# Kernel optimization log

Hardware: AMD Instinct MI355X
Metric: run time of the kernel (lower is better)

## Reference

```python
import jax, jax.numpy as jnp
from jax import lax
import numpy as np

# pywt db4 decomposition filters (8 taps)
DEC_LO = np.array([-0.010597401785069032, 0.0328830116668852, 0.030841381835560764,
                   -0.18703481171909309, -0.027983769416859854, 0.6308807679298589,
                   0.7148465705529157, 0.2303778133088965], dtype=np.float32)
DEC_HI = np.array([-0.2303778133088965, 0.7148465705529157, -0.6308807679298589,
                   -0.027983769416859854, 0.18703481171909309, 0.030841381835560764,
                   -0.0328830116668852, -0.010597401785069032], dtype=np.float32)

LEVELS = 5
POOL = 128       # adaptive pool size inside each WaveletLevelNet
LEVEL_HID = 128  # per-level net output dim
OUT_DIM = 512
BATCH, SIGLEN = 2048, 16384


def dwt_step(a, filt):
    """One DWT level. a: [B, n]; filt: [2, L] (dec_lo, dec_hi).
    pywt-style: symmetric pad, full convolution, downsample at odd indices.
    Output length = floor((n + L - 1)/2)."""
    L = filt.shape[-1]
    xp = jnp.pad(a, ((0, 0), (L - 2, L - 1)), mode='symmetric')[:, None, :]  # [B,1,n+2L-3]
    k = filt[:, ::-1][:, None, :]  # flip -> true convolution; [2,1,L]
    out = lax.conv_general_dilated(xp, k, (2,), 'VALID',
                                   dimension_numbers=('NCH', 'OIH', 'NCH'))  # [B,2,m]
    return out[:, 0, :], out[:, 1, :]  # cA, cD


def wavedec(x, levels):
    filt = jnp.stack([jnp.asarray(DEC_LO), jnp.asarray(DEC_HI)])
    a = x
    details = []
    for _ in range(levels):  # small fixed loop over levels
        a, d = dwt_step(a, filt)
        details.append(d)
    return [a] + details[::-1]  # [cA_L, cD_L, cD_{L-1}, ..., cD_1]


def adaptive_avg_pool(x, P):
    """torch AdaptiveAvgPool1d over last dim via cumsum segment means."""
    n = x.shape[-1]
    idx = np.arange(P)
    starts = (idx * n) // P
    ends = ((idx + 1) * n + P - 1) // P
    cs = jnp.cumsum(x, axis=-1)
    cs = jnp.concatenate([jnp.zeros_like(cs[..., :1]), cs], axis=-1)
    return (cs[..., ends] - cs[..., starts]) / jnp.asarray(ends - starts, x.dtype)


def setup_inputs() -> dict:
    key = jax.random.key(0)
    k0, k1, k2 = jax.random.split(key, 3)
    x = jax.random.normal(k0, (BATCH, SIGLEN), dtype=jnp.float32)
    level_w = jax.random.normal(k1, (LEVELS, LEVEL_HID, POOL), dtype=jnp.float32) * 0.05
    level_b = jnp.zeros((LEVELS, LEVEL_HID), dtype=jnp.float32)
    fusion_w = jax.random.normal(k2, (OUT_DIM, LEVELS * LEVEL_HID), dtype=jnp.float32) * 0.05
    fusion_b = jnp.zeros((OUT_DIM,), dtype=jnp.float32)
    return {"x": x, "level_w": level_w, "level_b": level_b,
            "fusion_w": fusion_w, "fusion_b": fusion_b}


def reference(x, level_w, level_b, fusion_w, fusion_b):
    coeffs = wavedec(x, LEVELS)  # 6 arrays; forward uses the first 5
    pooled = jnp.stack([adaptive_avg_pool(coeffs[i], POOL) for i in range(LEVELS)])  # [5,B,P]
    feats = jax.nn.relu(jnp.einsum('lbp,lop->lbo', pooled, level_w) + level_b[:, None, :])
    comb = jnp.transpose(feats, (1, 0, 2)).reshape(x.shape[0], LEVELS * LEVEL_HID)  # [B,640]
    return jax.nn.relu(comb @ fusion_w.T + fusion_b)  # Dropout is identity in eval
```

## Files before the change

kernel.cpp:

```cpp
#include <hip/hip_runtime.h>


#define BATCH   2048
#define SIGLEN  16384
#define N1      8195
#define N2      4101
#define N3      2054
#define N4      1030
#define N5      518
#define POOLP   128
#define COMB    640
#define OUTD    512
#define NTHR    512

#define LW_PAIRS (5 * 128 * 128 / 2)
#define FW_PAIRS (512 * 640 / 2)
#define PACK_BLOCKS ((LW_PAIRS + FW_PAIRS) / 256)

#define SWZ(i) ((i) ^ ((((i) >> 5) & 7) << 2))

typedef __fp16 h2 __attribute__((ext_vector_type(2)));
typedef float  f2 __attribute__((ext_vector_type(2)));

__device__ constexpr float LO[8] = {
     0.2303778133088965f,   0.7148465705529157f,   0.6308807679298589f,
    -0.027983769416859854f, -0.18703481171909309f,  0.030841381835560764f,
     0.0328830116668852f,  -0.010597401785069032f };
__device__ constexpr float HI[8] = {
    -0.010597401785069032f, -0.0328830116668852f,   0.030841381835560764f,
     0.18703481171909309f,  -0.027983769416859854f, -0.6308807679298589f,
     0.7148465705529157f,  -0.2303778133088965f };

__device__ __forceinline__ int symfold(int idx, int n) {
    idx = (idx < 0) ? (-1 - idx) : idx;
    idx = (idx >= n) ? (2 * n - 1 - idx) : idx;
    return idx;
}
constexpr int cmin(int a, int b) { return a < b ? a : b; }
constexpr int cmax(int a, int b) { return a > b ? a : b; }

template<int SS, int SE, int BSRC, int NSRC, int S, int E, int BDST>
__device__ __forceinline__ void dwt_chunk(const float* __restrict__ src,
                                          float* __restrict__ dstA,
                                          float* __restrict__ dstD, int tid) {
    for (int j0 = (S & ~3) + tid * 4; j0 < E; j0 += NTHR * 4) {
        const int rb = 2 * j0 - 8;
        if ((rb >= SS) && (2 * j0 + 7 <= SE - 1) && (j0 + 4 <= E)) {
            const int lrb = rb - BSRC;
            const float4 v0 = *reinterpret_cast<const float4*>(src + SWZ(lrb));
            const float4 v1 = *reinterpret_cast<const float4*>(src + SWZ(lrb + 4));
            const float4 v2 = *reinterpret_cast<const float4*>(src + SWZ(lrb + 8));
            const float4 v3 = *reinterpret_cast<const float4*>(src + SWZ(lrb + 12));
            float w[16];
            w[0]=v0.x;  w[1]=v0.y;  w[2]=v0.z;  w[3]=v0.w;
            w[4]=v1.x;  w[5]=v1.y;  w[6]=v1.z;  w[7]=v1.w;
            w[8]=v2.x;  w[9]=v2.y;  w[10]=v2.z; w[11]=v2.w;
            w[12]=v3.x; w[13]=v3.y; w[14]=v3.z; w[15]=v3.w;
            float a[4], d[4];
#pragma unroll
            for (int k = 0; k < 4; ++k) {
                f2 ad = {0.f, 0.f};
#pragma unroll
                for (int t = 0; t < 8; ++t) {
                    const float v = w[2 + 2 * k + t];
                    const f2 vv = {v, v};
                    const f2 lh = {LO[t], HI[t]};
                    ad = __builtin_elementwise_fma(vv, lh, ad);
                }
                a[k] = ad.x; d[k] = ad.y;
            }
            const int ds = j0 - BDST;
            *reinterpret_cast<float4*>(dstA + SWZ(ds)) = make_float4(a[0], a[1], a[2], a[3]);
            *reinterpret_cast<float4*>(dstD + SWZ(ds)) = make_float4(d[0], d[1], d[2], d[3]);
        } else {
            for (int k = 0; k < 4; ++k) {
                const int j = j0 + k;
                if (j < S || j >= E) continue;
                float aa = 0.f, dd = 0.f;
#pragma unroll
                for (int t = 0; t < 8; ++t) {
                    const int idx = symfold(2 * j - 6 + t, NSRC);
                    const float v = src[SWZ(idx - BSRC)];
                    aa = fmaf(v, LO[t], aa);
                    dd = fmaf(v, HI[t], dd);
                }
                dstA[SWZ(j - BDST)] = aa;
                dstD[SWZ(j - BDST)] = dd;
            }
        }
    }
}

template<int S, int E, int BDST>
__device__ __forceinline__ void dwt_l1(const float* __restrict__ xr,
                                       float* __restrict__ dstA, int tid) {
    for (int j0 = (S & ~3) + tid * 4; j0 < E; j0 += NTHR * 4) {
        const int rb = 2 * j0 - 8;
        if ((rb >= 0) && (2 * j0 + 7 <= SIGLEN - 1) && (j0 + 4 <= E)) {
            const float4* s4 = reinterpret_cast<const float4*>(xr + rb);
            const float4 v0 = s4[0], v1 = s4[1], v2 = s4[2], v3 = s4[3];
            float w[16];
            w[0]=v0.x;  w[1]=v0.y;  w[2]=v0.z;  w[3]=v0.w;
            w[4]=v1.x;  w[5]=v1.y;  w[6]=v1.z;  w[7]=v1.w;
            w[8]=v2.x;  w[9]=v2.y;  w[10]=v2.z; w[11]=v2.w;
            w[12]=v3.x; w[13]=v3.y; w[14]=v3.z; w[15]=v3.w;
            f2 a01 = {0.f, 0.f}, a23 = {0.f, 0.f};
#pragma unroll
            for (int t = 0; t < 8; ++t) {
                const f2 p01 = {w[2 + t], w[4 + t]};
                const f2 p23 = {w[6 + t], w[8 + t]};
                const f2 lt  = {LO[t], LO[t]};
                a01 = __builtin_elementwise_fma(p01, lt, a01);
                a23 = __builtin_elementwise_fma(p23, lt, a23);
            }
            *reinterpret_cast<float4*>(dstA + SWZ(j0 - BDST)) =
                make_float4(a01.x, a01.y, a23.x, a23.y);
        } else {
            for (int k = 0; k < 4; ++k) {
                const int j = j0 + k;
                if (j < S || j >= E) continue;
                float aa = 0.f;
#pragma unroll
                for (int t = 0; t < 8; ++t) {
                    const int idx = symfold(2 * j - 6 + t, SIGLEN);
                    aa = fmaf(xr[idx], LO[t], aa);
                }
                dstA[SWZ(j - BDST)] = aa;
            }
        }
    }
}

template<int N, int BASE, int P0>
__device__ __forceinline__ void pool64(const float* __restrict__ buf,
                                       __fp16* __restrict__ dst, int tid) {
    const int p = P0 + (tid >> 3), sub = tid & 7;
    const int s = (p * N) >> 7;
    const int e = ((p + 1) * N + 127) >> 7;
    float acc = 0.f;
    for (int t = s + sub; t < e; t += 8) acc += buf[SWZ(t - BASE)];
    acc += __shfl_xor(acc, 1);
    acc += __shfl_xor(acc, 2);
    acc += __shfl_xor(acc, 4);
    if (sub == 0) dst[p] = (__fp16)(acc / (float)(e - s));
}

template<int B>
__device__ __forceinline__ void dwt_body(const float* __restrict__ xr,
                                         __fp16* __restrict__ pr,
                                         float* __restrict__ A, float* __restrict__ Bb,
                                         float* __restrict__ D1, float* __restrict__ D2,
                                         int tid) {
    constexpr int p0 = B * 64;
    constexpr int sP5 = (p0 * N5) >> 7, eP5 = ((p0 + 64) * N5 + 127) >> 7;
    constexpr int sP4 = (p0 * N4) >> 7, eP4 = ((p0 + 64) * N4 + 127) >> 7;
    constexpr int sP3 = (p0 * N3) >> 7, eP3 = ((p0 + 64) * N3 + 127) >> 7;
    constexpr int sP2 = (p0 * N2) >> 7, eP2 = ((p0 + 64) * N2 + 127) >> 7;
    constexpr int s5 = sP5, e5 = cmin(eP5, N5);
    constexpr int s4 = cmax(cmin(sP4, 2 * s5 - 6), 0);
    constexpr int e4 = cmin(cmax(eP4, 2 * e5), N4);
    constexpr int s3 = cmax(cmin(sP3, 2 * s4 - 6), 0);
    constexpr int e3 = cmin(cmax(eP3, 2 * e4), N3);
    constexpr int s2 = cmax(cmin(sP2, 2 * s3 - 6), 0);
    constexpr int e2 = cmin(cmax(eP2, 2 * e3), N2);
    constexpr int s1 = cmax(2 * s2 - 6, 0);
    constexpr int e1 = cmin(2 * e2, N1);
    constexpr int b1 = (s1 & ~3) - 8, b2 = (s2 & ~3) - 8, b3 = (s3 & ~3) - 8;
    constexpr int b4 = (s4 & ~3) - 8, b5 = (s5 & ~3) - 8;

    dwt_l1<s1, e1, b1>(xr, A, tid);
    __syncthreads();
    dwt_chunk<s1, e1, b1, N1, s2, e2, b2>(A, Bb, D1, tid);
    __syncthreads();
    dwt_chunk<s2, e2, b2, N2, s3, e3, b3>(Bb, A, D2, tid);
    pool64<N2, b2, p0>(D1, pr + 4 * POOLP, tid);
    __syncthreads();
    dwt_chunk<s3, e3, b3, N3, s4, e4, b4>(A, Bb, D1, tid);
    pool64<N3, b3, p0>(D2, pr + 3 * POOLP, tid);
    __syncthreads();
    dwt_chunk<s4, e4, b4, N4, s5, e5, b5>(Bb, A, D2, tid);
    pool64<N4, b4, p0>(D1, pr + 2 * POOLP, tid);
    __syncthreads();
    pool64<N5, b5, p0>(A,  pr + 0 * POOLP, tid);
    pool64<N5, b5, p0>(D2, pr + 1 * POOLP, tid);
}

__global__ __launch_bounds__(NTHR, 4) void dwt_pool_kernel(const float* __restrict__ x,
                                                           __fp16* __restrict__ pooled,
                                                           const float* __restrict__ lw,
                                                           const float* __restrict__ fw,
                                                           h2* __restrict__ lwh,
                                                           h2* __restrict__ fwh) {
    __shared__ __align__(16) float A[4192];
    __shared__ __align__(16) float Bb[2144];
    __shared__ __align__(16) float D1[2144];
    __shared__ __align__(16) float D2[1088];
    const int tid = threadIdx.x;

    if (lwh != nullptr && blockIdx.x < PACK_BLOCKS && tid < 256) {
        const int i = blockIdx.x * 256 + tid;
        if (i < LW_PAIRS) {
            const float2 v = reinterpret_cast<const float2*>(lw)[i];
            lwh[i] = __builtin_amdgcn_cvt_pkrtz(v.x, v.y);
        } else {
            const float2 v = reinterpret_cast<const float2*>(fw)[i - LW_PAIRS];
            fwh[i - LW_PAIRS] = __builtin_amdgcn_cvt_pkrtz(v.x, v.y);
        }
    }

    const int row = blockIdx.x >> 1;
    const float* __restrict__ xr = x + (size_t)row * SIGLEN;
    __fp16* __restrict__ pr = pooled + (size_t)row * COMB;
    if (blockIdx.x & 1) dwt_body<1>(xr, pr, A, Bb, D1, D2, tid);
    else                dwt_body<0>(xr, pr, A, Bb, D1, D2, tid);
}


__global__ __launch_bounds__(1024, 4) void mlp_kernel(const __fp16* __restrict__ pooled,
                                                      const h2* __restrict__ lwh,
                                                      const float* __restrict__ lb,
                                                      const h2* __restrict__ fwh,
                                                      const float* __restrict__ fb,
                                                      float* __restrict__ out) {
    __shared__ h2 sph[8][COMB / 2];
    __shared__ h2 sch[8][COMB / 2];
    const int tid = threadIdx.x;
    const int r0 = blockIdx.x * 8;

    const h2* __restrict__ srcp = reinterpret_cast<const h2*>(pooled + (size_t)r0 * COMB);
    for (int i = tid; i < 8 * (COMB / 2); i += 1024) {
        (&sph[0][0])[i] = srcp[i];
    }
    __syncthreads();

    for (int idx = tid; idx < COMB * 2; idx += 1024) {
        const int c = idx >> 1, rh = (idx & 1) * 4;
        const h2* __restrict__ w = lwh + (size_t)c * 64;
        const int lb2 = (c >> 7) * 64;
        const float bias = lb[c];
        float acc[4] = {bias, bias, bias, bias};
        for (int t2 = 0; t2 < 64; t2 += 4) {
            const float4 wraw = *reinterpret_cast<const float4*>(w + t2);
            const h2 w0 = __builtin_bit_cast(h2, wraw.x);
            const h2 w1 = __builtin_bit_cast(h2, wraw.y);
            const h2 w2 = __builtin_bit_cast(h2, wraw.z);
            const h2 w3 = __builtin_bit_cast(h2, wraw.w);
#pragma unroll
            for (int r = 0; r < 4; ++r) {
                const float4 praw = *reinterpret_cast<const float4*>(&sph[rh + r][lb2 + t2]);
                acc[r] = __builtin_amdgcn_fdot2(__builtin_bit_cast(h2, praw.x), w0, acc[r], false);
                acc[r] = __builtin_amdgcn_fdot2(__builtin_bit_cast(h2, praw.y), w1, acc[r], false);
                acc[r] = __builtin_amdgcn_fdot2(__builtin_bit_cast(h2, praw.z), w2, acc[r], false);
                acc[r] = __builtin_amdgcn_fdot2(__builtin_bit_cast(h2, praw.w), w3, acc[r], false);
            }
        }
        __fp16* __restrict__ schf = reinterpret_cast<__fp16*>(&sch[0][0]);
#pragma unroll
        for (int r = 0; r < 4; ++r) schf[(rh + r) * COMB + c] = (__fp16)fmaxf(acc[r], 0.f);
    }
    __syncthreads();

    {
        const int c = tid >> 1, rh = (tid & 1) * 4;
        const h2* __restrict__ w = fwh + (size_t)c * (COMB / 2);
        const float bias = fb[c];
        float acc[4] = {bias, bias, bias, bias};
        for (int t2 = 0; t2 < COMB / 2; t2 += 4) {
            const float4 wraw = *reinterpret_cast<const float4*>(w + t2);
            const h2 w0 = __builtin_bit_cast(h2, wraw.x);
            const h2 w1 = __builtin_bit_cast(h2, wraw.y);
            const h2 w2 = __builtin_bit_cast(h2, wraw.z);
            const h2 w3 = __builtin_bit_cast(h2, wraw.w);
#pragma unroll
            for (int r = 0; r < 4; ++r) {
                const float4 craw = *reinterpret_cast<const float4*>(&sch[rh + r][t2]);
                acc[r] = __builtin_amdgcn_fdot2(__builtin_bit_cast(h2, craw.x), w0, acc[r], false);
                acc[r] = __builtin_amdgcn_fdot2(__builtin_bit_cast(h2, craw.y), w1, acc[r], false);
                acc[r] = __builtin_amdgcn_fdot2(__builtin_bit_cast(h2, craw.z), w2, acc[r], false);
                acc[r] = __builtin_amdgcn_fdot2(__builtin_bit_cast(h2, craw.w), w3, acc[r], false);
            }
        }
#pragma unroll
        for (int r = 0; r < 4; ++r) {
            out[(size_t)(r0 + rh + r) * OUTD + c] = fmaxf(acc[r], 0.f);
        }
    }
}

__global__ __launch_bounds__(512) void mlp_kernel_fb(const __fp16* __restrict__ pooled,
                                                     const float* __restrict__ lw,
                                                     const float* __restrict__ lb,
                                                     const float* __restrict__ fw,
                                                     const float* __restrict__ fb,
                                                     float* __restrict__ out) {
    __shared__ h2 sph[8][COMB / 2];
    __shared__ h2 sch[8][COMB / 2];
    const int tid = threadIdx.x;
    const int r0 = blockIdx.x * 8;
    const h2* __restrict__ srcp = reinterpret_cast<const h2*>(pooled + (size_t)r0 * COMB);
    for (int i = tid; i < 8 * (COMB / 2); i += 512) {
        (&sph[0][0])[i] = srcp[i];
    }
    __syncthreads();
    for (int c = tid; c < COMB; c += 512) {
        const float* __restrict__ w = lw + (size_t)c * POOLP;
        const int lb2 = (c >> 7) * (POOLP / 2);
        const float bias = lb[c];
        float acc[8];
#pragma unroll
        for (int r = 0; r < 8; ++r) acc[r] = bias;
        for (int t2 = 0; t2 < POOLP / 2; t2 += 4) {
            const float4 wa = *reinterpret_cast<const float4*>(w + t2 * 2);
            const float4 wb = *reinterpret_cast<const float4*>(w + t2 * 2 + 4);
            const h2 w0 = __builtin_amdgcn_cvt_pkrtz(wa.x, wa.y);
            const h2 w1 = __builtin_amdgcn_cvt_pkrtz(wa.z, wa.w);
            const h2 w2 = __builtin_amdgcn_cvt_pkrtz(wb.x, wb.y);
            const h2 w3 = __builtin_amdgcn_cvt_pkrtz(wb.z, wb.w);
#pragma unroll
            for (int r = 0; r < 8; ++r) {
                const float4 raw = *reinterpret_cast<const float4*>(&sph[r][lb2 + t2]);
                acc[r] = __builtin_amdgcn_fdot2(__builtin_bit_cast(h2, raw.x), w0, acc[r], false);
                acc[r] = __builtin_amdgcn_fdot2(__builtin_bit_cast(h2, raw.y), w1, acc[r], false);
                acc[r] = __builtin_amdgcn_fdot2(__builtin_bit_cast(h2, raw.z), w2, acc[r], false);
                acc[r] = __builtin_amdgcn_fdot2(__builtin_bit_cast(h2, raw.w), w3, acc[r], false);
            }
        }
        __fp16* __restrict__ schf = reinterpret_cast<__fp16*>(&sch[0][0]);
#pragma unroll
        for (int r = 0; r < 8; ++r) schf[r * COMB + c] = (__fp16)fmaxf(acc[r], 0.f);
    }
    __syncthreads();
    {
        const int j = tid;
        const float* __restrict__ w = fw + (size_t)j * COMB;
        const float bias = fb[j];
        float acc[8];
#pragma unroll
        for (int r = 0; r < 8; ++r) acc[r] = bias;
        for (int t2 = 0; t2 < COMB / 2; t2 += 4) {
            const float4 wa = *reinterpret_cast<const float4*>(w + t2 * 2);
            const float4 wb = *reinterpret_cast<const float4*>(w + t2 * 2 + 4);
            const h2 w0 = __builtin_amdgcn_cvt_pkrtz(wa.x, wa.y);
            const h2 w1 = __builtin_amdgcn_cvt_pkrtz(wa.z, wa.w);
            const h2 w2 = __builtin_amdgcn_cvt_pkrtz(wb.x, wb.y);
            const h2 w3 = __builtin_amdgcn_cvt_pkrtz(wb.z, wb.w);
#pragma unroll
            for (int r = 0; r < 8; ++r) {
                const float4 raw = *reinterpret_cast<const float4*>(&sch[r][t2]);
                acc[r] = __builtin_amdgcn_fdot2(__builtin_bit_cast(h2, raw.x), w0, acc[r], false);
                acc[r] = __builtin_amdgcn_fdot2(__builtin_bit_cast(h2, raw.y), w1, acc[r], false);
                acc[r] = __builtin_amdgcn_fdot2(__builtin_bit_cast(h2, raw.z), w2, acc[r], false);
                acc[r] = __builtin_amdgcn_fdot2(__builtin_bit_cast(h2, raw.w), w3, acc[r], false);
            }
        }
#pragma unroll
        for (int r = 0; r < 8; ++r) {
            out[(size_t)(r0 + r) * OUTD + j] = fmaxf(acc[r], 0.f);
        }
    }
}

extern "C" void kernel_launch(void* const* d_in, const int* in_sizes, int n_in,
                              void* d_out, int out_size, void* d_ws, size_t ws_size,
                              hipStream_t stream) {
    const float* x  = (const float*)d_in[0];
    const float* lw = (const float*)d_in[1];
    const float* lb = (const float*)d_in[2];
    const float* fw = (const float*)d_in[3];
    const float* fb = (const float*)d_in[4];
    float* out = (float*)d_out;

    char* base = (char*)d_ws;
    const size_t POOLED_B = (size_t)BATCH * COMB * 2;
    const size_t LWH_B    = (size_t)LW_PAIRS * 4;
    const size_t FWH_B    = (size_t)FW_PAIRS * 4;

    __fp16* pooled = (__fp16*)base;
    h2* lwh = (h2*)(base + POOLED_B);
    h2* fwh = (h2*)(base + POOLED_B + LWH_B);

    const bool packed = (ws_size >= POOLED_B + LWH_B + FWH_B);

    dwt_pool_kernel<<<BATCH * 2, NTHR, 0, stream>>>(x, pooled, lw, fw,
                                                    packed ? lwh : nullptr,
                                                    packed ? fwh : nullptr);

    if (packed) {
        mlp_kernel<<<BATCH / 8, 1024, 0, stream>>>(pooled, lwh, lb, fwh, fb, out);
    } else {
        mlp_kernel_fb<<<BATCH / 8, 512, 0, stream>>>(pooled, lw, lb, fw, fb, out);
    }
}
```

Before: 87.98 us.

## Fuse first two DWT levels into one 22-tap composite filter from global memory

Levels 1 and 2 of the wavelet decomposition are merged by precomputing composite 22-tap filters (LO*LO for approximation, HI*LO for detail) at stride 4. Level-2 coefficients are then computed straight from the global input, which drops the level-1 intermediate in shared memory and one barrier. The largest shared buffer shrinks, which could allow more blocks per CU. In exchange each output needs 22 taps instead of two passes of 8, so there are more loads per thread and more registers, and the edge path is more expensive because of nested symmetric folding.

```diff
diff --git a/kernel.cpp b/kernel.cpp
--- a/kernel.cpp
+++ b/kernel.cpp
@@ -31,6 +31,19 @@
      0.18703481171909309f,  -0.027983769416859854f, -0.6308807679298589f,
      0.7148465705529157f,  -0.2303778133088965f };
 
+struct C22 { float a[22]; float d[22]; };
+__device__ constexpr C22 mk_c22() {
+    C22 c{};
+    for (int k = 0; k < 22; ++k) { c.a[k] = 0.f; c.d[k] = 0.f; }
+    for (int s = 0; s < 8; ++s)
+        for (int u = 0; u < 8; ++u) {
+            c.a[2 * s + u] += LO[s] * LO[u];
+            c.d[2 * s + u] += HI[s] * LO[u];
+        }
+    return c;
+}
+__device__ constexpr C22 CW2 = mk_c22();
+
 __device__ __forceinline__ int symfold(int idx, int n) {
     idx = (idx < 0) ? (-1 - idx) : idx;
     idx = (idx >= n) ? (2 * n - 1 - idx) : idx;
@@ -38,6 +51,58 @@
 }
 constexpr int cmin(int a, int b) { return a < b ? a : b; }
 constexpr int cmax(int a, int b) { return a > b ? a : b; }
+
+template<int S, int E, int BDST>
+__device__ __forceinline__ void dwt_l12(const float* __restrict__ xr,
+                                        float* __restrict__ dstA,
+                                        float* __restrict__ dstD, int tid) {
+    for (int j0 = (S & ~3) + tid * 4; j0 < E; j0 += NTHR * 4) {
+        if ((j0 >= 8) && (j0 <= 4092) && (j0 + 4 <= E)) {
+            const float4* s4 = reinterpret_cast<const float4*>(xr + 4 * j0 - 20);
+            float w[36];
+#pragma unroll
+            for (int q = 0; q < 9; ++q) {
+                const float4 v = s4[q];
+                w[4 * q] = v.x; w[4 * q + 1] = v.y; w[4 * q + 2] = v.z; w[4 * q + 3] = v.w;
+            }
+            float a[4], d[4];
+#pragma unroll
+            for (int k = 0; k < 4; ++k) {
+                f2 ad = {0.f, 0.f};
+#pragma unroll
+                for (int t = 0; t < 22; ++t) {
+                    const float v = w[4 * k + 2 + t];
+                    const f2 vv = {v, v};
+                    const f2 cw = {CW2.a[t], CW2.d[t]};
+                    ad = __builtin_elementwise_fma(vv, cw, ad);
+                }
+                a[k] = ad.x; d[k] = ad.y;
+            }
+            const int ds = j0 - BDST;
+            *reinterpret_cast<float4*>(dstA + SWZ(ds)) = make_float4(a[0], a[1], a[2], a[3]);
+            *reinterpret_cast<float4*>(dstD + SWZ(ds)) = make_float4(d[0], d[1], d[2], d[3]);
+        } else {
+            for (int k = 0; k < 4; ++k) {
+                const int j = j0 + k;
+                if (j < S || j >= E) continue;
+                float aa = 0.f, dd = 0.f;
+#pragma unroll
+                for (int s = 0; s < 8; ++s) {
+                    const int i = symfold(2 * j - 6 + s, N1);
+                    float l1 = 0.f;
+#pragma unroll
+                    for (int u = 0; u < 8; ++u) {
+                        l1 = fmaf(xr[symfold(2 * i - 6 + u, SIGLEN)], LO[u], l1);
+                    }
+                    aa = fmaf(l1, LO[s], aa);
+                    dd = fmaf(l1, HI[s], dd);
+                }
+                dstA[SWZ(j - BDST)] = aa;
+                dstD[SWZ(j - BDST)] = dd;
+            }
+        }
+    }
+}
 
 template<int SS, int SE, int BSRC, int NSRC, int S, int E, int BDST>
 __device__ __forceinline__ void dwt_chunk(const float* __restrict__ src,
@@ -91,46 +156,6 @@
     }
 }
 
-template<int S, int E, int BDST>
-__device__ __forceinline__ void dwt_l1(const float* __restrict__ xr,
-                                       float* __restrict__ dstA, int tid) {
-    for (int j0 = (S & ~3) + tid * 4; j0 < E; j0 += NTHR * 4) {
-        const int rb = 2 * j0 - 8;
-        if ((rb >= 0) && (2 * j0 + 7 <= SIGLEN - 1) && (j0 + 4 <= E)) {
-            const float4* s4 = reinterpret_cast<const float4*>(xr + rb);
-            const float4 v0 = s4[0], v1 = s4[1], v2 = s4[2], v3 = s4[3];
-            float w[16];
-            w[0]=v0.x;  w[1]=v0.y;  w[2]=v0.z;  w[3]=v0.w;
-            w[4]=v1.x;  w[5]=v1.y;  w[6]=v1.z;  w[7]=v1.w;
-            w[8]=v2.x;  w[9]=v2.y;  w[10]=v2.z; w[11]=v2.w;
-            w[12]=v3.x; w[13]=v3.y; w[14]=v3.z; w[15]=v3.w;
-            f2 a01 = {0.f, 0.f}, a23 = {0.f, 0.f};
-#pragma unroll
-            for (int t = 0; t < 8; ++t) {
-                const f2 p01 = {w[2 + t], w[4 + t]};
-                const f2 p23 = {w[6 + t], w[8 + t]};
-                const f2 lt  = {LO[t], LO[t]};
-                a01 = __builtin_elementwise_fma(p01, lt, a01);
-                a23 = __builtin_elementwise_fma(p23, lt, a23);
-            }
-            *reinterpret_cast<float4*>(dstA + SWZ(j0 - BDST)) =
-                make_float4(a01.x, a01.y, a23.x, a23.y);
-        } else {
-            for (int k = 0; k < 4; ++k) {
-                const int j = j0 + k;
-                if (j < S || j >= E) continue;
-                float aa = 0.f;
-#pragma unroll
-                for (int t = 0; t < 8; ++t) {
-                    const int idx = symfold(2 * j - 6 + t, SIGLEN);
-                    aa = fmaf(xr[idx], LO[t], aa);
-                }
-                dstA[SWZ(j - BDST)] = aa;
-            }
-        }
-    }
-}
-
 template<int N, int BASE, int P0>
 __device__ __forceinline__ void pool64(const float* __restrict__ buf,
                                        __fp16* __restrict__ dst, int tid) {
@@ -163,14 +188,10 @@
     constexpr int e3 = cmin(cmax(eP3, 2 * e4), N3);
     constexpr int s2 = cmax(cmin(sP2, 2 * s3 - 6), 0);
     constexpr int e2 = cmin(cmax(eP2, 2 * e3), N2);
-    constexpr int s1 = cmax(2 * s2 - 6, 0);
-    constexpr int e1 = cmin(2 * e2, N1);
-    constexpr int b1 = (s1 & ~3) - 8, b2 = (s2 & ~3) - 8, b3 = (s3 & ~3) - 8;
+    constexpr int b2 = (s2 & ~3) - 8, b3 = (s3 & ~3) - 8;
     constexpr int b4 = (s4 & ~3) - 8, b5 = (s5 & ~3) - 8;
 
-    dwt_l1<s1, e1, b1>(xr, A, tid);
-    __syncthreads();
-    dwt_chunk<s1, e1, b1, N1, s2, e2, b2>(A, Bb, D1, tid);
+    dwt_l12<s2, e2, b2>(xr, Bb, D1, tid);
     __syncthreads();
     dwt_chunk<s2, e2, b2, N2, s3, e3, b3>(Bb, A, D2, tid);
     pool64<N2, b2, p0>(D1, pr + 4 * POOLP, tid);
@@ -191,7 +212,7 @@
                                                            const float* __restrict__ fw,
                                                            h2* __restrict__ lwh,
                                                            h2* __restrict__ fwh) {
-    __shared__ __align__(16) float A[4192];
+    __shared__ __align__(16) float A[1088];
     __shared__ __align__(16) float Bb[2144];
     __shared__ __align__(16) float D1[2144];
     __shared__ __align__(16) float D2[1088];
```

Measured after the change: 171.7 us. +95.1%, slower.
